# Kernel optimization log

Hardware: AMD Instinct MI355X
Metric: run time of the kernel (lower is better)

The kernel has to match this reference:

```python
import jax, jax.numpy as jnp
import numpy as np

H = 8
LN_EPS = 1e-5


def _layer_norm(t):
    # LayerNorm over last dim, no affine (elementwise_affine=False, bias=False)
    mu = jnp.mean(t, axis=-1, keepdims=True)
    var = jnp.var(t, axis=-1, keepdims=True)
    return (t - mu) / jnp.sqrt(var + LN_EPS)


def setup_inputs() -> dict:
    key = jax.random.key(0)
    ks = jax.random.split(key, 7)
    B, N, D, K = 2, 8192, 512, 32
    x = jax.random.normal(ks[0], (B, N, D), dtype=jnp.float32)
    idx = jax.random.randint(ks[1], (N, K), 0, N)
    s = 1.0 / np.sqrt(D)  # kaiming-ish init scale for stability
    Wq = jax.random.normal(ks[2], (D, D), dtype=jnp.float32) * s
    Wk = jax.random.normal(ks[3], (D, D), dtype=jnp.float32) * s
    Wv = jax.random.normal(ks[4], (D, D), dtype=jnp.float32) * s
    Wout = jax.random.normal(ks[5], (D, D), dtype=jnp.float32) * s
    bout = jnp.zeros((D,), dtype=jnp.float32)
    return {"x": x, "idx": idx, "Wq": Wq, "Wk": Wk, "Wv": Wv, "Wout": Wout, "bout": bout}


def reference(x, idx, Wq, Wk, Wv, Wout, bout):
    B, N, D = x.shape
    d_k = D // H

    def proj(W):
        # torch Linear: x @ W.T ; reshape to (B, H, N, d_k)
        return (x @ W.T).reshape(B, N, H, d_k).transpose(0, 2, 1, 3)

    Q, K, V = proj(Wq), proj(Wk), proj(Wv)
    # per-head LayerNorm on d_k (all heads identical since no affine params)
    Q = _layer_norm(Q)
    K = _layer_norm(K)

    # grouped (neighborhood) attention: gather K,V at neighbor indices
    Kg = K[:, :, idx]  # (B, H, N, k, d_k)
    Vg = V[:, :, idx]  # (B, H, N, k, d_k)
    scores = jnp.einsum('bhnd,bhnkd->bhnk', Q, Kg) / jnp.sqrt(jnp.asarray(d_k, x.dtype))
    attn = jax.nn.softmax(scores, axis=-1)
    out = jnp.einsum('bhnk,bhnkd->bhnd', attn, Vg)  # (B, H, N, d_k)

    out = out.transpose(0, 2, 1, 3).reshape(B, N, D)
    return out @ Wout.T + bout
```

## Files before the change

### kernel.cpp

```cpp
#include <hip/hip_runtime.h>
#include <hip/hip_bf16.h>
#include <math.h>

#define BB 2
#define NN 8192
#define DD 512
#define HH 8
#define DK 64
#define KNB 32
#define BN (BB*NN)
#define BHN (BB*HH*NN)

typedef __attribute__((ext_vector_type(8))) _Float16 f16x8;
typedef __attribute__((ext_vector_type(2))) _Float16 f16x2;
typedef __attribute__((ext_vector_type(4))) float f32x4;

#if __has_builtin(__builtin_amdgcn_fdot2)
#define HAS_FDOT2 1
#endif

__device__ __forceinline__ unsigned short f2h(float f) {
    return __builtin_bit_cast(unsigned short, (_Float16)f);
}
__device__ __forceinline__ f16x2 u2h2(unsigned u) {
    return __builtin_bit_cast(f16x2, u);
}
__device__ __forceinline__ float h2f_lo(unsigned u) {
    return (float)__builtin_bit_cast(_Float16, (unsigned short)(u & 0xffffu));
}
__device__ __forceinline__ float h2f_hi(unsigned u) {
    return (float)__builtin_bit_cast(_Float16, (unsigned short)(u >> 16));
}
__device__ __forceinline__ float dot2h(unsigned a, unsigned b, float c) {
#ifdef HAS_FDOT2
    return __builtin_amdgcn_fdot2(u2h2(a), u2h2(b), c, false);
#else
    c = fmaf(h2f_lo(a), h2f_lo(b), c);
    return fmaf(h2f_hi(a), h2f_hi(b), c);
#endif
}

__device__ __forceinline__ void gload_lds16(const void* gptr, void* lptr) {
    __builtin_amdgcn_global_load_lds(
        (const __attribute__((address_space(1))) unsigned int*)gptr,
        (__attribute__((address_space(3))) unsigned int*)lptr,
        16, 0, 0);
}

__global__ __launch_bounds__(256) void cvt_all(
    const float* __restrict__ x,
    const float* __restrict__ Wq, const float* __restrict__ Wk,
    const float* __restrict__ Wv, const float* __restrict__ Wo,
    unsigned short* __restrict__ Xb, unsigned short* __restrict__ Wfb,
    unsigned short* __restrict__ Wob)
{
    const int blk = blockIdx.x;
    const float* src;
    unsigned short* dst;
    int off;
    if (blk < 8192) {
        off = (blk * 256 + threadIdx.x) * 4;
        src = x; dst = Xb;
    } else {
        const int e = ((blk - 8192) * 256 + threadIdx.x) * 4;
        const int t = e >> 18;
        off = e & 262143;
        src = (t == 0) ? Wq : (t == 1) ? Wk : (t == 2) ? Wv : Wo;
        dst = (t < 3) ? (Wfb + (size_t)t * 262144) : Wob;
    }
    const float4 v = *(const float4*)(src + off);
    ushort4 u;
    u.x = f2h(v.x); u.y = f2h(v.y); u.z = f2h(v.z); u.w = f2h(v.w);
    *(ushort4*)(dst + off) = u;
}

__global__ __launch_bounds__(256) void gemm_qkv(
    const unsigned short* __restrict__ Xb, const unsigned short* __restrict__ Wfb,
    unsigned short* __restrict__ Qh, unsigned short* __restrict__ Kh,
    unsigned short* __restrict__ Vh)
{
    __shared__ unsigned short Als[128 * 32];
    __shared__ unsigned short Bls[128 * 32];
    const int tid  = threadIdx.x;
    const int wave = tid >> 6, lane = tid & 63;
    const int wm = wave >> 1, wn = wave & 1;
    const int quad = lane >> 4, r = lane & 15;
    const int row0 = blockIdx.x * 128;
    const int c0   = blockIdx.y * 128;

    f32x4 acc[4][4];
    #pragma unroll
    for (int i = 0; i < 4; ++i)
        #pragma unroll
        for (int j = 0; j < 4; ++j) acc[i][j] = (f32x4)0.f;

    const char* Ab = (const char*)Xb;
    const char* Bb = (const char*)Wfb;

    for (int k0 = 0; k0 < 512; k0 += 32) {
        __syncthreads();
        #pragma unroll
        for (int q = 0; q < 2; ++q) {
            const int li = q * 4096 + wave * 1024 + lane * 16;
            const int rr = li >> 6, off = li & 63;
            gload_lds16(Ab + (size_t)(row0 + rr) * 1024 + k0 * 2 + off,
                        (char*)Als + (q * 4096 + wave * 1024));
            gload_lds16(Bb + (size_t)(c0 + rr) * 1024 + k0 * 2 + off,
                        (char*)Bls + (q * 4096 + wave * 1024));
        }
        __syncthreads();

        f16x8 af[4], bf[4];
        #pragma unroll
        for (int i = 0; i < 4; ++i)
            af[i] = *(const f16x8*)(&Als[(wm * 64 + i * 16 + r) * 32 + quad * 8]);
        #pragma unroll
        for (int j = 0; j < 4; ++j)
            bf[j] = *(const f16x8*)(&Bls[(wn * 64 + j * 16 + r) * 32 + quad * 8]);
        #pragma unroll
        for (int i = 0; i < 4; ++i)
            #pragma unroll
            for (int j = 0; j < 4; ++j)
                acc[i][j] = __builtin_amdgcn_mfma_f32_16x16x32_f16(af[i], bf[j], acc[i][j], 0, 0, 0);
    }

    const int tensor = c0 >> 9;
    unsigned short* OutH = (tensor == 0) ? Qh : (tensor == 1) ? Kh : Vh;

    float mu[4][4], rs[4][4];
    if (tensor < 2) {
        #pragma unroll
        for (int i = 0; i < 4; ++i) {
            #pragma unroll
            for (int reg = 0; reg < 4; ++reg) {
                float sm = acc[i][0][reg] + acc[i][1][reg] + acc[i][2][reg] + acc[i][3][reg];
                sm += __shfl_xor(sm, 1); sm += __shfl_xor(sm, 2);
                sm += __shfl_xor(sm, 4); sm += __shfl_xor(sm, 8);
                const float muv = sm * (1.f / 64.f);
                float qv = 0.f;
                #pragma unroll
                for (int j = 0; j < 4; ++j) {
                    const float dv = acc[i][j][reg] - muv;
                    qv = fmaf(dv, dv, qv);
                }
                qv += __shfl_xor(qv, 1); qv += __shfl_xor(qv, 2);
                qv += __shfl_xor(qv, 4); qv += __shfl_xor(qv, 8);
                mu[i][reg] = muv;
                rs[i][reg] = rsqrtf(qv * (1.f / 64.f) + 1e-5f);
            }
        }
    }

    #pragma unroll
    for (int i = 0; i < 4; ++i) {
        #pragma unroll
        for (int j = 0; j < 4; ++j) {
            const int cc = (c0 & 511) + wn * 64 + j * 16 + r;
            const int h = cc >> 6, d = cc & 63;
            #pragma unroll
            for (int reg = 0; reg < 4; ++reg) {
                const int row = row0 + wm * 64 + i * 16 + quad * 4 + reg;
                const int b = row >> 13, n = row & 8191;
                float v = acc[i][j][reg];
                if (tensor < 2) v = (v - mu[i][reg]) * rs[i][reg];
                OutH[(((size_t)(b * HH + h) * NN + n) << 6) + d] = f2h(v);
            }
        }
    }
}

__global__ __launch_bounds__(256, 2) void attn(
    const unsigned short* __restrict__ Qh, const unsigned short* __restrict__ Kh,
    const unsigned short* __restrict__ Vh,
    const int* __restrict__ idx, unsigned short* __restrict__ Ob)
{
    const int p = blockIdx.x;
    const int L = ((p & 7) << 12) | (p >> 3);
    const int wave = threadIdx.x >> 6;
    const int wid  = L * 4 + wave;
    const int lane = threadIdx.x & 63;
    const int bh = wid >> 13;
    const int n  = wid & 8191;
    const size_t base = (size_t)bh * NN * DK;

    const int g_all = idx[n * KNB + (lane & 31)];

    const int k    = lane >> 1;
    const int half = lane & 1;
    const int g    = __builtin_amdgcn_ds_bpermute(k * 4, g_all);

    const uint4* q4 = (const uint4*)(Qh + base + ((size_t)n << 6) + half * 32);
    const uint4* k4 = (const uint4*)(Kh + base + ((size_t)g << 6) + half * 32);
    float a0 = 0.f, a1 = 0.f;
    {
        const uint4 qa = q4[0], ka = k4[0];
        a0 = dot2h(qa.x, ka.x, a0); a0 = dot2h(qa.y, ka.y, a0);
        a0 = dot2h(qa.z, ka.z, a0); a0 = dot2h(qa.w, ka.w, a0);
    }
    {
        const uint4 qa = q4[1], ka = k4[1];
        a1 = dot2h(qa.x, ka.x, a1); a1 = dot2h(qa.y, ka.y, a1);
        a1 = dot2h(qa.z, ka.z, a1); a1 = dot2h(qa.w, ka.w, a1);
    }
    {
        const uint4 qa = q4[2], ka = k4[2];
        a0 = dot2h(qa.x, ka.x, a0); a0 = dot2h(qa.y, ka.y, a0);
        a0 = dot2h(qa.z, ka.z, a0); a0 = dot2h(qa.w, ka.w, a0);
    }
    {
        const uint4 qa = q4[3], ka = k4[3];
        a1 = dot2h(qa.x, ka.x, a1); a1 = dot2h(qa.y, ka.y, a1);
        a1 = dot2h(qa.z, ka.z, a1); a1 = dot2h(qa.w, ka.w, a1);
    }
    const float acc = a0 + a1;
    const float s = (acc + __shfl_xor(acc, 1)) * 0.125f;

    const float e = __expf(s);
    float tot = e;
    #pragma unroll
    for (int off = 2; off <= 32; off <<= 1) tot += __shfl_xor(tot, off);
    const float pr = e / tot;

    const unsigned prh = (unsigned)f2h(pr);
    const unsigned pp = prh | (((unsigned)__shfl_xor((int)prh, 2)) << 16);

    const char* Vbytes = (const char*)Vh + (base << 1);
    const int c2 = lane & 31, h2 = lane >> 5;
    float o0 = 0.f, o1 = 0.f;
    #pragma unroll
    for (int j = 0; j < 8; ++j) {
        const int r0 = __builtin_amdgcn_ds_bpermute((h2 * 16 + 2 * j) * 4, g_all);
        const int r1 = __builtin_amdgcn_ds_bpermute((h2 * 16 + 2 * j + 1) * 4, g_all);
        const unsigned vx = *(const unsigned*)(Vbytes + (size_t)(r0 * 128) + c2 * 4);
        const unsigned vy = *(const unsigned*)(Vbytes + (size_t)(r1 * 128) + c2 * 4);
        const unsigned ppj = (unsigned)__builtin_amdgcn_ds_bpermute(h2 * 128 + j * 16, (int)pp);
        const unsigned t0 = __builtin_amdgcn_perm(vx, vy, 0x01000504u);
        const unsigned t1 = __builtin_amdgcn_perm(vx, vy, 0x03020706u);
        o0 = dot2h(t0, ppj, o0);
        o1 = dot2h(t1, ppj, o1);
    }
    o0 += __shfl_xor(o0, 32);
    o1 += __shfl_xor(o1, 32);
    if (lane < 32) {
        const int b = bh >> 3, hh = bh & 7;
        const unsigned ov = (unsigned)f2h(o0) | ((unsigned)f2h(o1) << 16);
        *(unsigned*)(Ob + ((size_t)(b * NN + n)) * DD + hh * DK + 2 * c2) = ov;
    }
}

__global__ __launch_bounds__(256) void gemm_out(
    const unsigned short* __restrict__ Ob, const unsigned short* __restrict__ Wob,
    const float* __restrict__ bout, float* __restrict__ out)
{
    __shared__ unsigned short Als[128 * 32];
    __shared__ unsigned short Bls[128 * 32];
    const int tid  = threadIdx.x;
    const int wave = tid >> 6, lane = tid & 63;
    const int wm = wave >> 1, wn = wave & 1;
    const int quad = lane >> 4, r = lane & 15;
    const int row0 = blockIdx.x * 128;
    const int c0   = blockIdx.y * 128;

    f32x4 acc[4][4];
    #pragma unroll
    for (int i = 0; i < 4; ++i)
        #pragma unroll
        for (int j = 0; j < 4; ++j) acc[i][j] = (f32x4)0.f;

    const char* Ab = (const char*)Ob;
    const char* Bb = (const char*)Wob;

    for (int k0 = 0; k0 < 512; k0 += 32) {
        __syncthreads();
        #pragma unroll
        for (int q = 0; q < 2; ++q) {
            const int li = q * 4096 + wave * 1024 + lane * 16;
            const int rr = li >> 6, off = li & 63;
            gload_lds16(Ab + (size_t)(row0 + rr) * 1024 + k0 * 2 + off,
                        (char*)Als + (q * 4096 + wave * 1024));
            gload_lds16(Bb + (size_t)(c0 + rr) * 1024 + k0 * 2 + off,
                        (char*)Bls + (q * 4096 + wave * 1024));
        }
        __syncthreads();

        f16x8 af[4], bf[4];
        #pragma unroll
        for (int i = 0; i < 4; ++i)
            af[i] = *(const f16x8*)(&Als[(wm * 64 + i * 16 + r) * 32 + quad * 8]);
        #pragma unroll
        for (int j = 0; j < 4; ++j)
            bf[j] = *(const f16x8*)(&Bls[(wn * 64 + j * 16 + r) * 32 + quad * 8]);
        #pragma unroll
        for (int i = 0; i < 4; ++i)
            #pragma unroll
            for (int j = 0; j < 4; ++j)
                acc[i][j] = __builtin_amdgcn_mfma_f32_16x16x32_f16(af[i], bf[j], acc[i][j], 0, 0, 0);
    }

    #pragma unroll
    for (int i = 0; i < 4; ++i) {
        #pragma unroll
        for (int j = 0; j < 4; ++j) {
            const int colg = c0 + wn * 64 + j * 16 + r;
            const float bb = bout[colg];
            #pragma unroll
            for (int reg = 0; reg < 4; ++reg) {
                const int row = row0 + wm * 64 + i * 16 + quad * 4 + reg;
                out[((size_t)row << 9) + colg] = acc[i][j][reg] + bb;
            }
        }
    }
}

extern "C" void kernel_launch(void* const* d_in, const int* in_sizes, int n_in,
                              void* d_out, int out_size, void* d_ws, size_t ws_size,
                              hipStream_t stream)
{
    const float* x    = (const float*)d_in[0];
    const int*   idx  = (const int*)  d_in[1];
    const float* Wq   = (const float*)d_in[2];
    const float* Wk   = (const float*)d_in[3];
    const float* Wv   = (const float*)d_in[4];
    const float* Wout = (const float*)d_in[5];
    const float* bout = (const float*)d_in[6];

    char* ws = (char*)d_ws;
    unsigned short* Qh  = (unsigned short*)(ws);
    unsigned short* Kh  = (unsigned short*)(ws + 16777216);
    unsigned short* Vh  = (unsigned short*)(ws + 33554432);
    unsigned short* Xb  = (unsigned short*)(ws + 50331648);
    unsigned short* Ob  = Xb;
    unsigned short* Wfb = (unsigned short*)(ws + 67108864);
    unsigned short* Wob = (unsigned short*)(ws + 68681728);
    float* out = (float*)d_out;

    cvt_all<<<9216, 256, 0, stream>>>(x, Wq, Wk, Wv, Wout, Xb, Wfb, Wob);

    dim3 g1(BN / 128, 1536 / 128);
    gemm_qkv<<<g1, 256, 0, stream>>>(Xb, Wfb, Qh, Kh, Vh);

    attn<<<BHN / 4, 256, 0, stream>>>(Qh, Kh, Vh, idx, Ob);

    dim3 g2(BN / 128, 512 / 128);
    gemm_out<<<g2, 256, 0, stream>>>(Ob, Wob, bout, out);
}
```

Measured before the change: 219.8 us.

## Double-buffer LDS in GEMMs and remap blocks across XCDs

Both the QKV and output GEMMs now double-buffer their LDS tiles, so the global-to-LDS loads for the next K step are issued before the MFMAs on the current step, with one barrier per iteration instead of two. The 2D grid is flattened to 1D and remapped so that consecutive logical tiles sharing the same row block land on the same XCD, aiming for better L2 reuse. This doubles LDS use per block, which may reduce occupancy.

```diff
diff --git a/kernel.cpp b/kernel.cpp
--- a/kernel.cpp
+++ b/kernel.cpp
@@ -79,14 +79,16 @@
     unsigned short* __restrict__ Qh, unsigned short* __restrict__ Kh,
     unsigned short* __restrict__ Vh)
 {
-    __shared__ unsigned short Als[128 * 32];
-    __shared__ unsigned short Bls[128 * 32];
+    __shared__ unsigned short Als[2][128 * 32];
+    __shared__ unsigned short Bls[2][128 * 32];
     const int tid  = threadIdx.x;
     const int wave = tid >> 6, lane = tid & 63;
     const int wm = wave >> 1, wn = wave & 1;
     const int quad = lane >> 4, r = lane & 15;
-    const int row0 = blockIdx.x * 128;
-    const int c0   = blockIdx.y * 128;
+    const int p = blockIdx.x;
+    const int L = (p & 7) * 192 + (p >> 3);
+    const int row0 = (L / 12) * 128;
+    const int c0   = (L % 12) * 128;
 
     f32x4 acc[4][4];
     #pragma unroll
@@ -97,31 +99,43 @@
     const char* Ab = (const char*)Xb;
     const char* Bb = (const char*)Wfb;
 
-    for (int k0 = 0; k0 < 512; k0 += 32) {
-        __syncthreads();
-        #pragma unroll
-        for (int q = 0; q < 2; ++q) {
-            const int li = q * 4096 + wave * 1024 + lane * 16;
-            const int rr = li >> 6, off = li & 63;
-            gload_lds16(Ab + (size_t)(row0 + rr) * 1024 + k0 * 2 + off,
-                        (char*)Als + (q * 4096 + wave * 1024));
-            gload_lds16(Bb + (size_t)(c0 + rr) * 1024 + k0 * 2 + off,
-                        (char*)Bls + (q * 4096 + wave * 1024));
-        }
-        __syncthreads();
+    const int li0 = wave * 1024 + lane * 16;
+    const int rr0 = li0 >> 6, off0 = li0 & 63;
+    const int li1 = 4096 + li0;
+    const int rr1 = li1 >> 6, off1 = li1 & 63;
+
+    {
+        gload_lds16(Ab + (size_t)(row0 + rr0) * 1024 + off0, (char*)Als[0] + (wave * 1024));
+        gload_lds16(Bb + (size_t)(c0   + rr0) * 1024 + off0, (char*)Bls[0] + (wave * 1024));
+        gload_lds16(Ab + (size_t)(row0 + rr1) * 1024 + off1, (char*)Als[0] + (4096 + wave * 1024));
+        gload_lds16(Bb + (size_t)(c0   + rr1) * 1024 + off1, (char*)Bls[0] + (4096 + wave * 1024));
+    }
+    __syncthreads();
+
+    for (int kt = 0; kt < 16; ++kt) {
+        const int cur = kt & 1;
+        if (kt < 15) {
+            const int kb = (kt + 1) * 64;
+            gload_lds16(Ab + (size_t)(row0 + rr0) * 1024 + kb + off0, (char*)Als[cur ^ 1] + (wave * 1024));
+            gload_lds16(Bb + (size_t)(c0   + rr0) * 1024 + kb + off0, (char*)Bls[cur ^ 1] + (wave * 1024));
+            gload_lds16(Ab + (size_t)(row0 + rr1) * 1024 + kb + off1, (char*)Als[cur ^ 1] + (4096 + wave * 1024));
+            gload_lds16(Bb + (size_t)(c0   + rr1) * 1024 + kb + off1, (char*)Bls[cur ^ 1] + (4096 + wave * 1024));
+        }
 
         f16x8 af[4], bf[4];
         #pragma unroll
         for (int i = 0; i < 4; ++i)
-            af[i] = *(const f16x8*)(&Als[(wm * 64 + i * 16 + r) * 32 + quad * 8]);
+            af[i] = *(const f16x8*)(&Als[cur][(wm * 64 + i * 16 + r) * 32 + quad * 8]);
         #pragma unroll
         for (int j = 0; j < 4; ++j)
-            bf[j] = *(const f16x8*)(&Bls[(wn * 64 + j * 16 + r) * 32 + quad * 8]);
+            bf[j] = *(const f16x8*)(&Bls[cur][(wn * 64 + j * 16 + r) * 32 + quad * 8]);
         #pragma unroll
         for (int i = 0; i < 4; ++i)
             #pragma unroll
             for (int j = 0; j < 4; ++j)
                 acc[i][j] = __builtin_amdgcn_mfma_f32_16x16x32_f16(af[i], bf[j], acc[i][j], 0, 0, 0);
+
+        __syncthreads();
     }
 
     const int tensor = c0 >> 9;
@@ -252,14 +266,16 @@
     const unsigned short* __restrict__ Ob, const unsigned short* __restrict__ Wob,
     const float* __restrict__ bout, float* __restrict__ out)
 {
-    __shared__ unsigned short Als[128 * 32];
-    __shared__ unsigned short Bls[128 * 32];
+    __shared__ unsigned short Als[2][128 * 32];
+    __shared__ unsigned short Bls[2][128 * 32];
     const int tid  = threadIdx.x;
     const int wave = tid >> 6, lane = tid & 63;
     const int wm = wave >> 1, wn = wave & 1;
     const int quad = lane >> 4, r = lane & 15;
-    const int row0 = blockIdx.x * 128;
-    const int c0   = blockIdx.y * 128;
+    const int p = blockIdx.x;
+    const int L = (p & 7) * 64 + (p >> 3);
+    const int row0 = (L >> 2) * 128;
+    const int c0   = (L & 3) * 128;
 
     f32x4 acc[4][4];
     #pragma unroll
@@ -270,31 +286,43 @@
     const char* Ab = (const char*)Ob;
     const char* Bb = (const char*)Wob;
 
-    for (int k0 = 0; k0 < 512; k0 += 32) {
-        __syncthreads();
-        #pragma unroll
-        for (int q = 0; q < 2; ++q) {
-            const int li = q * 4096 + wave * 1024 + lane * 16;
-            const int rr = li >> 6, off = li & 63;
-            gload_lds16(Ab + (size_t)(row0 + rr) * 1024 + k0 * 2 + off,
-                        (char*)Als + (q * 4096 + wave * 1024));
-            gload_lds16(Bb + (size_t)(c0 + rr) * 1024 + k0 * 2 + off,
-                        (char*)Bls + (q * 4096 + wave * 1024));
-        }
-        __syncthreads();
+    const int li0 = wave * 1024 + lane * 16;
+    const int rr0 = li0 >> 6, off0 = li0 & 63;
+    const int li1 = 4096 + li0;
+    const int rr1 = li1 >> 6, off1 = li1 & 63;
+
+    {
+        gload_lds16(Ab + (size_t)(row0 + rr0) * 1024 + off0, (char*)Als[0] + (wave * 1024));
+        gload_lds16(Bb + (size_t)(c0   + rr0) * 1024 + off0, (char*)Bls[0] + (wave * 1024));
+        gload_lds16(Ab + (size_t)(row0 + rr1) * 1024 + off1, (char*)Als[0] + (4096 + wave * 1024));
+        gload_lds16(Bb + (size_t)(c0   + rr1) * 1024 + off1, (char*)Bls[0] + (4096 + wave * 1024));
+    }
+    __syncthreads();
+
+    for (int kt = 0; kt < 16; ++kt) {
+        const int cur = kt & 1;
+        if (kt < 15) {
+            const int kb = (kt + 1) * 64;
+            gload_lds16(Ab + (size_t)(row0 + rr0) * 1024 + kb + off0, (char*)Als[cur ^ 1] + (wave * 1024));
+            gload_lds16(Bb + (size_t)(c0   + rr0) * 1024 + kb + off0, (char*)Bls[cur ^ 1] + (wave * 1024));
+            gload_lds16(Ab + (size_t)(row0 + rr1) * 1024 + kb + off1, (char*)Als[cur ^ 1] + (4096 + wave * 1024));
+            gload_lds16(Bb + (size_t)(c0   + rr1) * 1024 + kb + off1, (char*)Bls[cur ^ 1] + (4096 + wave * 1024));
+        }
 
         f16x8 af[4], bf[4];
         #pragma unroll
         for (int i = 0; i < 4; ++i)
-            af[i] = *(const f16x8*)(&Als[(wm * 64 + i * 16 + r) * 32 + quad * 8]);
+            af[i] = *(const f16x8*)(&Als[cur][(wm * 64 + i * 16 + r) * 32 + quad * 8]);
         #pragma unroll
         for (int j = 0; j < 4; ++j)
-            bf[j] = *(const f16x8*)(&Bls[(wn * 64 + j * 16 + r) * 32 + quad * 8]);
+            bf[j] = *(const f16x8*)(&Bls[cur][(wn * 64 + j * 16 + r) * 32 + quad * 8]);
         #pragma unroll
         for (int i = 0; i < 4; ++i)
             #pragma unroll
             for (int j = 0; j < 4; ++j)
                 acc[i][j] = __builtin_amdgcn_mfma_f32_16x16x32_f16(af[i], bf[j], acc[i][j], 0, 0, 0);
+
+        __syncthreads();
     }
 
     #pragma unroll
@@ -336,11 +364,9 @@
 
     cvt_all<<<9216, 256, 0, stream>>>(x, Wq, Wk, Wv, Wout, Xb, Wfb, Wob);
 
-    dim3 g1(BN / 128, 1536 / 128);
-    gemm_qkv<<<g1, 256, 0, stream>>>(Xb, Wfb, Qh, Kh, Vh);
+    gemm_qkv<<<1536, 256, 0, stream>>>(Xb, Wfb, Qh, Kh, Vh);
 
     attn<<<BHN / 4, 256, 0, stream>>>(Qh, Kh, Vh, idx, Ob);
 
-    dim3 g2(BN / 128, 512 / 128);
-    gemm_out<<<g2, 256, 0, stream>>>(Ob, Wob, bout, out);
-}
+    gemm_out<<<512, 256, 0, stream>>>(Ob, Wob, bout, out);
+}
```

Result: no change. 221.2 us (+0.6%).
